# Performance work log

Hardware: AMD Instinct MI355X
Metric: run time of the kernel (lower is better)

## Reference

```python
import jax, jax.numpy as jnp
import numpy as np

H = 768
NH = 12
HD = H // NH
FF = 3072
EPS = 1e-5
CHUNK = 32  # query chunk for L1 distance to bound memory


def layer_norm(x, g, b):
    mu = jnp.mean(x, axis=-1, keepdims=True)
    var = jnp.mean((x - mu) ** 2, axis=-1, keepdims=True)
    return (x - mu) / jnp.sqrt(var + EPS) * g + b


def l1_distance(Q, K):
    # Q, K: [BH, S, D] -> [BH, S, S], computed in query chunks to avoid
    # materializing the full [BH, S, S, D] broadcast intermediate.
    BH, S, D = Q.shape
    nc = S // CHUNK
    Qc = Q.reshape(BH, nc, CHUNK, D).transpose(1, 0, 2, 3)  # [nc, BH, c, D]

    def f(qc):  # qc: [BH, c, D]
        return jnp.sum(jnp.abs(qc[:, :, None, :] - K[:, None, :, :]), axis=-1)

    d = jax.lax.map(f, Qc)  # [nc, BH, c, S]
    return d.transpose(1, 0, 2, 3).reshape(BH, S, S)


def setup_inputs() -> dict:
    key = jax.random.key(0)
    ks = jax.random.split(key, 12)
    sd = 0.02
    B, S = 2, 1024
    return {
        'hidden_states': jax.random.normal(ks[0], (B, S, H), jnp.float32),
        'ln1_g': jnp.ones((H,), jnp.float32),
        'ln1_b': jnp.zeros((H,), jnp.float32),
        'Wq': jax.random.normal(ks[1], (H, H), jnp.float32) * sd,
        'bq': jnp.zeros((H,), jnp.float32),
        'Wk': jax.random.normal(ks[2], (H, H), jnp.float32) * sd,
        'bk': jnp.zeros((H,), jnp.float32),
        'Wv': jax.random.normal(ks[3], (H, H), jnp.float32) * sd,
        'bv': jnp.zeros((H,), jnp.float32),
        'Wo': jax.random.normal(ks[4], (H, H), jnp.float32) * sd,
        'bo': jnp.zeros((H,), jnp.float32),
        'lam': jnp.asarray(1.0, jnp.float32),
        'ln2_g': jnp.ones((H,), jnp.float32),
        'ln2_b': jnp.zeros((H,), jnp.float32),
        'W1': jax.random.normal(ks[5], (H, FF), jnp.float32) * sd,
        'b1': jnp.zeros((FF,), jnp.float32),
        'W2': jax.random.normal(ks[6], (FF, H), jnp.float32) * sd,
        'b2': jnp.zeros((H,), jnp.float32),
    }


def reference(hidden_states, ln1_g, ln1_b, Wq, bq, Wk, bk, Wv, bv, Wo, bo,
              lam, ln2_g, ln2_b, W1, b1, W2, b2):
    B, S, _ = hidden_states.shape
    scale = 1.0 / np.sqrt(HD)

    residual = hidden_states
    x = layer_norm(hidden_states, ln1_g, ln1_b)

    Q = (x @ Wq + bq).reshape(B, S, NH, HD).transpose(0, 2, 1, 3)  # [B,H,S,D]
    K = (x @ Wk + bk).reshape(B, S, NH, HD).transpose(0, 2, 1, 3)
    V = (x @ Wv + bv).reshape(B, S, NH, HD).transpose(0, 2, 1, 3)

    Qf = Q.reshape(B * NH, S, HD)
    Kf = K.reshape(B * NH, S, HD)
    dist = l1_distance(Qf, Kf).reshape(B, NH, S, S)

    scores = -lam * dist * scale
    attn = jax.nn.softmax(scores, axis=-1)  # [B,H,S,S]

    out = jnp.einsum('bhqk,bhkd->bhqd', attn, V)
    out = out.transpose(0, 2, 1, 3).reshape(B, S, H)
    out = out @ Wo + bo
    out = residual + out

    residual = out
    y = layer_norm(out, ln2_g, ln2_b)
    y = jax.nn.gelu(y @ W1 + b1, approximate=False) @ W2 + b2
    out = residual + y
    return out, attn
```

## Files before the change

### kernel.cpp

```cpp
#include <hip/hip_runtime.h>
#include <cstdint>
#include <cstddef>

#define SB    1024
#define BB    2
#define HH    768
#define NHH   12
#define HDD   64
#define FFF   3072
#define RR    (BB*SB)
#define NQKV  2304

#define QSCALE 42.5f

typedef __attribute__((ext_vector_type(8))) short short8;
typedef __attribute__((ext_vector_type(4))) float f4;

__device__ __forceinline__ unsigned short f2bf(float f) {
  union { float f; unsigned u; } x; x.f = f;
  unsigned r = x.u + 0x7FFFu + ((x.u >> 16) & 1u);
  return (unsigned short)(r >> 16);
}

__device__ __forceinline__ unsigned qz8(float x) {
  int v = (int)rintf(x * QSCALE) + 128;
  v = v < 0 ? 0 : (v > 255 ? 255 : v);
  return (unsigned)v;
}

__device__ __forceinline__ void async16(void* lds, const void* g) {
  __builtin_amdgcn_global_load_lds((const __attribute__((address_space(1))) unsigned int*)g,
                                   (__attribute__((address_space(3))) unsigned int*)lds,
                                   16, 0, 0);
}

__global__ __launch_bounds__(256)
void prep_all(const float* __restrict__ Wq, const float* __restrict__ Wk,
              const float* __restrict__ Wv, const float* __restrict__ Wo,
              const float* __restrict__ W1, const float* __restrict__ W2,
              const float* __restrict__ bq, const float* __restrict__ bk,
              const float* __restrict__ bv,
              const float* __restrict__ hidden, const float* __restrict__ ln1_g,
              const float* __restrict__ ln1_b,
              unsigned short* __restrict__ Wqkv_t, unsigned short* __restrict__ W1t,
              unsigned short* __restrict__ W2t, float* __restrict__ bqkv,
              unsigned short* __restrict__ xb) {
  const int t = blockIdx.x;
  const int tid = threadIdx.x;
  __shared__ float tile[64][65];
  __shared__ float rs[4], rq[4];
  if (t >= 1737) {
    const int row = t - 1737;
    const float* x = hidden + (size_t)row * HH;
    float v0 = x[tid], v1 = x[tid + 256], v2 = x[tid + 512];
    float s = v0 + v1 + v2;
    float q = v0 * v0 + v1 * v1 + v2 * v2;
    #pragma unroll
    for (int o = 32; o >= 1; o >>= 1) { s += __shfl_xor(s, o); q += __shfl_xor(q, o); }
    const int w = tid >> 6;
    if ((tid & 63) == 0) { rs[w] = s; rq[w] = q; }
    __syncthreads();
    s = rs[0] + rs[1] + rs[2] + rs[3];
    q = rq[0] + rq[1] + rq[2] + rq[3];
    float mean = s * (1.0f / HH);
    float rstd = rsqrtf(q * (1.0f / HH) - mean * mean + 1e-5f);
    unsigned short* o0 = xb + (size_t)row * HH;
    o0[tid]       = f2bf((v0 - mean) * rstd * ln1_g[tid]       + ln1_b[tid]);
    o0[tid + 256] = f2bf((v1 - mean) * rstd * ln1_g[tid + 256] + ln1_b[tid + 256]);
    o0[tid + 512] = f2bf((v2 - mean) * rstd * ln1_g[tid + 512] + ln1_b[tid + 512]);
    return;
  }
  if (t >= 1728) {
    int i = (t - 1728) * 256 + tid;
    if (i < NQKV)
      bqkv[i] = (i < HH) ? bq[i] : (i < 2 * HH ? bk[i - HH] : bv[i - 2 * HH]);
    return;
  }
  const float* in; unsigned short* out; int ldin, ldout, r0, c0;
  if (t < 576) {
    int m = t / 144, q = t % 144;
    in = m == 0 ? Wq : (m == 1 ? Wk : (m == 2 ? Wv : Wo));
    out = Wqkv_t + (size_t)m * HH * HH;
    ldin = HH; ldout = HH;
    r0 = (q / 12) * 64; c0 = (q % 12) * 64;
  } else if (t < 1152) {
    int q = t - 576;
    in = W1; out = W1t; ldin = FFF; ldout = HH;
    r0 = (q % 12) * 64; c0 = (q / 12) * 64;
  } else {
    int q = t - 1152;
    in = W2; out = W2t; ldin = HH; ldout = FFF;
    r0 = (q % 48) * 64; c0 = (q / 48) * 64;
  }
  for (int i = tid; i < 4096; i += 256) {
    int r = i >> 6, c = i & 63;
    tile[r][c] = in[(size_t)(r0 + r) * ldin + c0 + c];
  }
  __syncthreads();
  for (int i = tid; i < 4096; i += 256) {
    int cc = i >> 6, rr = i & 63;
    out[(size_t)(c0 + cc) * ldout + r0 + rr] = f2bf(tile[rr][cc]);
  }
}

__global__ __launch_bounds__(256)
void gemm_qkv(const unsigned short* __restrict__ A, const unsigned short* __restrict__ Bt,
              const float* __restrict__ bqkv, unsigned* __restrict__ Qq,
              unsigned* __restrict__ Kq, unsigned short* __restrict__ Vt) {
  __shared__ __align__(16) unsigned char smem[49152];
  unsigned short (*lA)[128 * 32] = (unsigned short (*)[128 * 32])smem;
  unsigned short (*lB)[128 * 32] = (unsigned short (*)[128 * 32])(smem + 24576);
  const unsigned short* Ab = A + (size_t)blockIdx.y * 128 * HH;
  const unsigned short* Bb = Bt + (size_t)blockIdx.x * 128 * HH;
  const int tid = threadIdx.x;
  const int wave = tid >> 6, lane = tid & 63;
  const int wr = wave >> 1, wc = wave & 1;
  const int lo = lane & 15, hi = lane >> 4;

  auto stage = [&](int k0, int buf) {
    #pragma unroll
    for (int i = 0; i < 512; i += 256) {
      int idx = i + tid; int r = idx >> 2, kg = idx & 3;
      async16(&lA[buf][idx * 8], &Ab[(size_t)r * HH + k0 + kg * 8]);
    }
    #pragma unroll
    for (int i = 0; i < 512; i += 256) {
      int idx = i + tid; int r = idx >> 2, kg = idx & 3;
      async16(&lB[buf][idx * 8], &Bb[(size_t)r * HH + k0 + kg * 8]);
    }
  };

  stage(0, 0);
  stage(32, 1);
  f4 acc[4][4] = {};
  for (int it = 0; it < 24; it++) {
    if (it + 1 < 24) {
      asm volatile("s_waitcnt vmcnt(4)" ::: "memory");
    } else {
      asm volatile("s_waitcnt vmcnt(0)" ::: "memory");
    }
    __builtin_amdgcn_s_barrier();
    __builtin_amdgcn_sched_barrier(0);
    const int cur = it % 3;
    short8 af[4], bf[4];
    #pragma unroll
    for (int i = 0; i < 4; i++)
      af[i] = *(const short8*)&lA[cur][(wr * 64 + i * 16 + lo) * 32 + hi * 8];
    #pragma unroll
    for (int j = 0; j < 4; j++)
      bf[j] = *(const short8*)&lB[cur][(wc * 64 + j * 16 + lo) * 32 + hi * 8];
    if (it + 2 < 24) stage((it + 2) * 32, (it + 2) % 3);
    #pragma unroll
    for (int i = 0; i < 4; i++)
      #pragma unroll
      for (int j = 0; j < 4; j++)
        acc[i][j] = __builtin_amdgcn_mfma_f32_16x16x32_bf16(af[i], bf[j], acc[i][j], 0, 0, 0);
  }
  __syncthreads();

  const int reg = blockIdx.x / 6;
  const int cb = blockIdx.x * 128;
  if (reg < 2) {
    unsigned char* t8 = smem;
    #pragma unroll
    for (int i = 0; i < 4; i++)
      #pragma unroll
      for (int j = 0; j < 4; j++) {
        int col = wc * 64 + j * 16 + lo;
        float bv_ = bqkv[cb + col];
        #pragma unroll
        for (int r = 0; r < 4; r++) {
          int row = wr * 64 + i * 16 + hi * 4 + r;
          t8[row * 132 + col] = (unsigned char)qz8(acc[i][j][r] + bv_);
        }
      }
    __syncthreads();
    const unsigned* t32 = (const unsigned*)smem;
    if (reg == 0) {
      #pragma unroll
      for (int i0 = 0; i0 < 4096; i0 += 256) {
        int idx = i0 + tid;
        int cw = idx & 31, rw = idx >> 5;
        int token = blockIdx.y * 128 + rw;
        Qq[(size_t)token * 192 + blockIdx.x * 32 + cw] = t32[rw * 33 + cw];
      }
    } else {
      #pragma unroll
      for (int i0 = 0; i0 < 4096; i0 += 256) {
        int idx = i0 + tid;
        int rw = idx & 127, cw = idx >> 7;
        int token = blockIdx.y * 128 + rw;
        int b = token >> 10, k = token & 1023;
        int dgG = (blockIdx.x - 6) * 32 + cw;
        Kq[(size_t)((b * NHH + (dgG >> 4)) * 16 + (dgG & 15)) * SB + k] = t32[rw * 33 + cw];
      }
    }
  } else {
    unsigned short* t16 = (unsigned short*)smem;
    #pragma unroll
    for (int i = 0; i < 4; i++)
      #pragma unroll
      for (int j = 0; j < 4; j++) {
        int col = wc * 64 + j * 16 + lo;
        float bv_ = bqkv[cb + col];
        #pragma unroll
        for (int r = 0; r < 4; r++) {
          int row = wr * 64 + i * 16 + hi * 4 + r;
          t16[col * 130 + row] = f2bf(acc[i][j][r] + bv_);
        }
      }
    __syncthreads();
    const unsigned* tv = (const unsigned*)smem;
    unsigned* VtU = (unsigned*)Vt;
    #pragma unroll
    for (int i0 = 0; i0 < 8192; i0 += 256) {
      int idx = i0 + tid;
      int rp = idx & 63, cw = idx >> 6;
      int gcol = (blockIdx.x - 12) * 128 + cw;
      int h = gcol >> 6, d = gcol & 63;
      int b = blockIdx.y >> 3;
      VtU[(size_t)((b * NHH + h) * HDD + d) * 512 + (blockIdx.y & 7) * 64 + rp] =
          tv[cw * 65 + rp];
    }
  }
}

template<int BM, int BN, int WR, int WC, int MODE, int KS>
__global__ __launch_bounds__(WR*WC*64)
void gemm_bt(const unsigned short* __restrict__ A, int ldA,
             const unsigned short* __restrict__ Bt, int ldB,
             void* __restrict__ Cv, int ldC,
             const float* __restrict__ bias,
             int K, long partStride) {
  constexpr int T = WR * WC * 64;
  constexpr int LPT = (BM * 4 + BN * 4) / T;
  __shared__ unsigned short lA[3][BM * 32];
  __shared__ unsigned short lB[3][BN * 32];
  const int ks = blockIdx.z;
  const int KH = K / KS;
  const unsigned short* Ab = A + (size_t)blockIdx.y * BM * ldA + (size_t)ks * KH;
  const unsigned short* Bb = Bt + (size_t)blockIdx.x * BN * ldB + (size_t)ks * KH;
  const long cOff = (long)blockIdx.y * BM * ldC + (long)blockIdx.x * BN
                  + (long)ks * partStride;
  const int tid = threadIdx.x;
  const int wave = tid >> 6, lane = tid & 63;
  const int wr = wave / WC, wc = wave % WC;
  const int lo = lane & 15, hi = lane >> 4;

  auto stage = [&](int k0, int buf) {
    #pragma unroll
    for (int i = 0; i < BM * 4; i += T) {
      int idx = i + tid; int r = idx >> 2, kg = idx & 3;
      async16(&lA[buf][idx * 8], &Ab[(size_t)r * ldA + k0 + kg * 8]);
    }
    #pragma unroll
    for (int i = 0; i < BN * 4; i += T) {
      int idx = i + tid; int r = idx >> 2, kg = idx & 3;
      async16(&lB[buf][idx * 8], &Bb[(size_t)r * ldB + k0 + kg * 8]);
    }
  };

  const int nIter = KH / 32;
  stage(0, 0);
  if (nIter > 1) stage(32, 1);
  f4 acc[4][4] = {};
  for (int it = 0; it < nIter; it++) {
    if (it + 1 < nIter) {
      asm volatile("s_waitcnt vmcnt(%0)" :: "n"(LPT) : "memory");
    } else {
      asm volatile("s_waitcnt vmcnt(0)" ::: "memory");
    }
    __builtin_amdgcn_s_barrier();
    __builtin_amdgcn_sched_barrier(0);
    const int cur = it % 3;
    short8 af[4], bf[4];
    #pragma unroll
    for (int i = 0; i < 4; i++)
      af[i] = *(const short8*)&lA[cur][(wr * 64 + i * 16 + lo) * 32 + hi * 8];
    #pragma unroll
    for (int j = 0; j < 4; j++)
      bf[j] = *(const short8*)&lB[cur][(wc * 64 + j * 16 + lo) * 32 + hi * 8];
    if (it + 2 < nIter) stage((it + 2) * 32, (it + 2) % 3);
    #pragma unroll
    for (int i = 0; i < 4; i++)
      #pragma unroll
      for (int j = 0; j < 4; j++)
        acc[i][j] = __builtin_amdgcn_mfma_f32_16x16x32_bf16(af[i], bf[j], acc[i][j], 0, 0, 0);
  }
  float* Cf = (float*)Cv;
  unsigned short* Cb = (unsigned short*)Cv;
  const int bc0 = blockIdx.x * BN;
  #pragma unroll
  for (int i = 0; i < 4; i++) {
    #pragma unroll
    for (int j = 0; j < 4; j++) {
      int col = wc * 64 + j * 16 + lo;
      #pragma unroll
      for (int r = 0; r < 4; r++) {
        int row = wr * 64 + i * 16 + hi * 4 + r;
        size_t idx = (size_t)cOff + (size_t)row * ldC + col;
        float v = acc[i][j][r];
        if constexpr (MODE == 3) {
          float tt = v + bias[bc0 + col];
          Cb[idx] = f2bf(0.5f * tt * (1.0f + erff(tt * 0.70710678118654752f)));
        } else {
          Cf[idx] = v;
        }
      }
    }
  }
}

__global__ __launch_bounds__(256)
void reduce_ln(const float* __restrict__ p, const float* __restrict__ bias,
               const float* __restrict__ res, const float* __restrict__ g,
               const float* __restrict__ bb, float* __restrict__ attnOut,
               unsigned short* __restrict__ out) {
  const int row = blockIdx.x, tid = threadIdx.x;
  const size_t rb = (size_t)row * HH;
  float v[3]; float s = 0.f, q = 0.f;
  #pragma unroll
  for (int j = 0; j < 3; j++) {
    int c = tid + j * 256;
    size_t idx = rb + c;
    float a = p[idx] + p[(size_t)RR * HH + idx] + p[2 * (size_t)RR * HH + idx]
            + p[3 * (size_t)RR * HH + idx] + bias[c] + res[idx];
    attnOut[idx] = a;
    v[j] = a; s += a; q += a * a;
  }
  #pragma unroll
  for (int o = 32; o >= 1; o >>= 1) { s += __shfl_xor(s, o); q += __shfl_xor(q, o); }
  __shared__ float rs[4], rq[4];
  const int w = tid >> 6;
  if ((tid & 63) == 0) { rs[w] = s; rq[w] = q; }
  __syncthreads();
  s = rs[0] + rs[1] + rs[2] + rs[3];
  q = rq[0] + rq[1] + rq[2] + rq[3];
  float mean = s * (1.0f / HH);
  float rstd = rsqrtf(q * (1.0f / HH) - mean * mean + 1e-5f);
  #pragma unroll
  for (int j = 0; j < 3; j++) {
    int c = tid + j * 256;
    out[rb + c] = f2bf((v[j] - mean) * rstd * g[c] + bb[c]);
  }
}

__global__ __launch_bounds__(256)
void reduce4_bias_res(const float* __restrict__ p, const float* __restrict__ bias,
                      const float* __restrict__ res, float* __restrict__ out) {
  int i = (blockIdx.x * 256 + threadIdx.x) * 4;
  int col = i % HH;
  float4 a = *(const float4*)(p + i);
  #pragma unroll
  for (int s = 1; s < 4; s++) {
    float4 b = *(const float4*)(p + (size_t)s * RR * HH + i);
    a.x += b.x; a.y += b.y; a.z += b.z; a.w += b.w;
  }
  float4 bb = *(const float4*)(bias + col);
  float4 r = *(const float4*)(res + i);
  float4 o;
  o.x = a.x + bb.x + r.x;
  o.y = a.y + bb.y + r.y;
  o.z = a.z + bb.z + r.z;
  o.w = a.w + bb.w + r.w;
  *(float4*)(out + i) = o;
}

#define DQ 16
__global__ __launch_bounds__(512)
void dist_softmax_pv(const unsigned* __restrict__ Qq, const unsigned* __restrict__ Kq,
                     const unsigned short* __restrict__ Vt,
                     const float* __restrict__ lam_p,
                     float* __restrict__ attnF, unsigned short* __restrict__ ctx) {
  __shared__ __align__(16) unsigned lk[8 * SB];
  __shared__ unsigned lq[DQ * 16];
  const int bh = blockIdx.y;
  const int q0 = blockIdx.x * DQ;
  const int b = bh / NHH, h = bh % NHH;
  const int tid = threadIdx.x;
  const int w = tid >> 6, lane = tid & 63;
  const int lo = lane & 15, hi = lane >> 4;

  if (tid < 256) {
    int r = tid >> 4, dg = tid & 15;
    lq[r * 16 + dg] = Qq[(size_t)(b * SB + q0 + r) * 192 + h * 16 + dg];
  }

  const unsigned* Ks = Kq + (size_t)bh * 16 * SB;
  unsigned acc[2][4][4] = {};
  const unsigned* lqw = &lq[(w * 2) * 16];

  #pragma unroll
  for (int ch = 0; ch < 2; ch++) {
    #pragma unroll
    for (int i = 0; i < 4; i++)
      async16(&lk[(i * 512 + tid) * 4], Ks + (size_t)ch * 8192 + (i * 512 + tid) * 4);
    __syncthreads();
    #pragma unroll
    for (int dg = 0; dg < 8; dg++) {
      unsigned qd[2];
      #pragma unroll
      for (int qi = 0; qi < 2; qi++) qd[qi] = lqw[qi * 16 + ch * 8 + dg];
      uint4 kv[4];
      #pragma unroll
      for (int kg = 0; kg < 4; kg++)
        kv[kg] = *(const uint4*)&lk[dg * SB + kg * 256 + lane * 4];
      #pragma unroll
      for (int qi = 0; qi < 2; qi++) {
        #pragma unroll
        for (int kg = 0; kg < 4; kg++) {
          acc[qi][kg][0] = __builtin_amdgcn_sad_u8(qd[qi], kv[kg].x, acc[qi][kg][0]);
          acc[qi][kg][1] = __builtin_amdgcn_sad_u8(qd[qi], kv[kg].y, acc[qi][kg][1]);
          acc[qi][kg][2] = __builtin_amdgcn_sad_u8(qd[qi], kv[kg].z, acc[qi][kg][2]);
          acc[qi][kg][3] = __builtin_amdgcn_sad_u8(qd[qi], kv[kg].w, acc[qi][kg][3]);
        }
      }
    }
    __syncthreads();
  }

  unsigned short* lp = (unsigned short*)lk;
  const float kscl = -lam_p[0] * 0.125f / QSCALE;
  #pragma unroll
  for (int qi = 0; qi < 2; qi++) {
    float sc[16];
    float m = -1e30f;
    #pragma unroll
    for (int kg = 0; kg < 4; kg++)
      #pragma unroll
      for (int c = 0; c < 4; c++) {
        float v = (float)acc[qi][kg][c] * kscl;
        sc[kg * 4 + c] = v;
        m = fmaxf(m, v);
      }
    #pragma unroll
    for (int off = 1; off < 64; off <<= 1) m = fmaxf(m, __shfl_xor(m, off));
    float s = 0.f;
    #pragma unroll
    for (int i = 0; i < 16; i++) {
      float e = __expf(sc[i] - m);
      sc[i] = e;
      s += e;
    }
    #pragma unroll
    for (int off = 1; off < 64; off <<= 1) s += __shfl_xor(s, off);
    const float rinv = 1.0f / s;
    const int row = w * 2 + qi;
    const size_t gb = (size_t)bh * SB * SB + (size_t)(q0 + row) * SB + lane * 4;
    #pragma unroll
    for (int kg = 0; kg < 4; kg++) {
      float4 p;
      p.x = sc[kg * 4 + 0] * rinv;
      p.y = sc[kg * 4 + 1] * rinv;
      p.z = sc[kg * 4 + 2] * rinv;
      p.w = sc[kg * 4 + 3] * rinv;
      *(float4*)&attnF[gb + kg * 256] = p;
      ushort4 pb;
      pb.x = f2bf(p.x); pb.y = f2bf(p.y); pb.z = f2bf(p.z); pb.w = f2bf(p.w);
      *(ushort4*)&lp[row * SB + kg * 256 + lane * 4] = pb;
    }
  }
  __syncthreads();

  if (w < 4) {
    const unsigned short* Vb = Vt + ((size_t)bh * HDD + w * 16 + lo) * SB + hi * 8;
    const unsigned short* Pb = lp + lo * SB + hi * 8;
    f4 cacc = {0.f, 0.f, 0.f, 0.f};
    #pragma unroll
    for (int k0 = 0; k0 < SB; k0 += 32) {
      short8 af = *(const short8*)(Pb + k0);
      short8 bf = *(const short8*)(Vb + k0);
      cacc = __builtin_amdgcn_mfma_f32_16x16x32_bf16(af, bf, cacc, 0, 0, 0);
    }
    unsigned short* cb = ctx + (size_t)(b * SB + q0 + hi * 4) * HH + h * HDD + w * 16 + lo;
    #pragma unroll
    for (int r = 0; r < 4; r++) cb[(size_t)r * HH] = f2bf(cacc[r]);
  }
}

extern "C" void kernel_launch(void* const* d_in, const int* in_sizes, int n_in,
                              void* d_out, int out_size, void* d_ws, size_t ws_size,
                              hipStream_t stream) {
  (void)in_sizes; (void)n_in; (void)out_size; (void)ws_size;
  const float* hidden = (const float*)d_in[0];
  const float* ln1_g  = (const float*)d_in[1];
  const float* ln1_b  = (const float*)d_in[2];
  const float* Wq     = (const float*)d_in[3];
  const float* bq     = (const float*)d_in[4];
  const float* Wk     = (const float*)d_in[5];
  const float* bk     = (const float*)d_in[6];
  const float* Wv     = (const float*)d_in[7];
  const float* bv     = (const float*)d_in[8];
  const float* Wo     = (const float*)d_in[9];
  const float* bo     = (const float*)d_in[10];
  const float* lam    = (const float*)d_in[11];
  const float* ln2_g  = (const float*)d_in[12];
  const float* ln2_b  = (const float*)d_in[13];
  const float* W1     = (const float*)d_in[14];
  const float* b1     = (const float*)d_in[15];
  const float* W2     = (const float*)d_in[16];
  const float* b2     = (const float*)d_in[17];

  float* out0  = (float*)d_out;
  float* attnF = out0 + (size_t)RR * HH;

  char* w = (char*)d_ws;
  auto alloc = [&](size_t bytes) { char* p = w; w += (bytes + 255) & ~(size_t)255; return p; };
  unsigned short* xb      = (unsigned short*)alloc((size_t)RR * HH * 2);
  unsigned short* Wqkv_t  = (unsigned short*)alloc((size_t)NQKV * HH * 2);
  unsigned short* Wo_t    = (unsigned short*)alloc((size_t)HH * HH * 2);
  unsigned short* W1t     = (unsigned short*)alloc((size_t)FFF * HH * 2);
  unsigned short* W2t     = (unsigned short*)alloc((size_t)HH * FFF * 2);
  float*          bqkv    = (float*)alloc((size_t)NQKV * 4);
  unsigned*       Qq      = (unsigned*)alloc((size_t)RR * 192 * 4);
  unsigned*       Kq      = (unsigned*)alloc((size_t)BB * NHH * 16 * SB * 4);
  unsigned short* Vt      = (unsigned short*)alloc((size_t)BB * NHH * HDD * SB * 2);
  unsigned short* ctx     = (unsigned short*)alloc((size_t)RR * HH * 2);
  float*          attnOut = (float*)alloc((size_t)RR * HH * 4);
  unsigned short* h1      = (unsigned short*)alloc((size_t)RR * FFF * 2);
  float*          gPart   = (float*)alloc((size_t)4 * RR * HH * 4);
  unsigned short* y2      = Vt;
  (void)Wo_t;

  prep_all<<<dim3(1737 + RR), 256, 0, stream>>>(Wq, Wk, Wv, Wo, W1, W2, bq, bk, bv,
                                                hidden, ln1_g, ln1_b,
                                                Wqkv_t, W1t, W2t, bqkv, xb);

  gemm_qkv<<<dim3(NQKV / 128, RR / 128), 256, 0, stream>>>(
      xb, Wqkv_t, bqkv, Qq, Kq, Vt);

  dist_softmax_pv<<<dim3(SB / DQ, BB * NHH), 512, 0, stream>>>(
      Qq, Kq, Vt, lam, attnF, ctx);

  gemm_bt<128, 128, 2, 2, 4, 4><<<dim3(HH / 128, RR / 128, 4), 256, 0, stream>>>(
      ctx, HH, Wqkv_t + (size_t)3 * HH * HH, HH, gPart, HH,
      nullptr, HH, (long)RR * HH);

  reduce_ln<<<dim3(RR), 256, 0, stream>>>(gPart, bo, hidden, ln2_g, ln2_b,
                                          attnOut, y2);

  gemm_bt<128, 128, 2, 2, 3, 1><<<dim3(FFF / 128, RR / 128, 1), 256, 0, stream>>>(
      y2, HH, W1t, HH, h1, FFF, b1, HH, 0);

  gemm_bt<128, 128, 2, 2, 4, 4><<<dim3(HH / 128, RR / 128, 4), 256, 0, stream>>>(
      h1, FFF, W2t, FFF, gPart, HH, nullptr, FFF, (long)RR * HH);

  reduce4_bias_res<<<dim3(RR * HH / 1024), 256, 0, stream>>>(gPart, b2, attnOut, out0);
}
```

Measured before the change: 283.5 us.

## Replace split-K partial buffers and reduction kernels with atomic accumulation into outputs

Result: slower. 302.0 us (+6.5%).

```diff
diff --git a/kernel.cpp b/kernel.cpp
--- a/kernel.cpp
+++ b/kernel.cpp
@@ -39,12 +39,12 @@
               const float* __restrict__ Wv, const float* __restrict__ Wo,
               const float* __restrict__ W1, const float* __restrict__ W2,
               const float* __restrict__ bq, const float* __restrict__ bk,
-              const float* __restrict__ bv,
+              const float* __restrict__ bv, const float* __restrict__ bo,
               const float* __restrict__ hidden, const float* __restrict__ ln1_g,
               const float* __restrict__ ln1_b,
               unsigned short* __restrict__ Wqkv_t, unsigned short* __restrict__ W1t,
               unsigned short* __restrict__ W2t, float* __restrict__ bqkv,
-              unsigned short* __restrict__ xb) {
+              unsigned short* __restrict__ xb, float* __restrict__ attnOut) {
   const int t = blockIdx.x;
   const int tid = threadIdx.x;
   __shared__ float tile[64][65];
@@ -53,6 +53,10 @@
     const int row = t - 1737;
     const float* x = hidden + (size_t)row * HH;
     float v0 = x[tid], v1 = x[tid + 256], v2 = x[tid + 512];
+    float* ao = attnOut + (size_t)row * HH;
+    ao[tid]       = v0 + bo[tid];
+    ao[tid + 256] = v1 + bo[tid + 256];
+    ao[tid + 512] = v2 + bo[tid + 512];
     float s = v0 + v1 + v2;
     float q = v0 * v0 + v1 * v1 + v2 * v2;
     #pragma unroll
@@ -231,7 +235,7 @@
              const unsigned short* __restrict__ Bt, int ldB,
              void* __restrict__ Cv, int ldC,
              const float* __restrict__ bias,
-             int K, long partStride) {
+             int K) {
   constexpr int T = WR * WC * 64;
   constexpr int LPT = (BM * 4 + BN * 4) / T;
   __shared__ unsigned short lA[3][BM * 32];
@@ -240,8 +244,7 @@
   const int KH = K / KS;
   const unsigned short* Ab = A + (size_t)blockIdx.y * BM * ldA + (size_t)ks * KH;
   const unsigned short* Bb = Bt + (size_t)blockIdx.x * BN * ldB + (size_t)ks * KH;
-  const long cOff = (long)blockIdx.y * BM * ldC + (long)blockIdx.x * BN
-                  + (long)ks * partStride;
+  const long cOff = (long)blockIdx.y * BM * ldC + (long)blockIdx.x * BN;
   const int tid = threadIdx.x;
   const int wave = tid >> 6, lane = tid & 63;
   const int wr = wave / WC, wc = wave % WC;
@@ -304,7 +307,7 @@
           float tt = v + bias[bc0 + col];
           Cb[idx] = f2bf(0.5f * tt * (1.0f + erff(tt * 0.70710678118654752f)));
         } else {
-          Cf[idx] = v;
+          atomicAdd(&Cf[idx], v);
         }
       }
     }
@@ -312,22 +315,18 @@
 }
 
 __global__ __launch_bounds__(256)
-void reduce_ln(const float* __restrict__ p, const float* __restrict__ bias,
-               const float* __restrict__ res, const float* __restrict__ g,
-               const float* __restrict__ bb, float* __restrict__ attnOut,
-               unsigned short* __restrict__ out) {
+void ln_b2(const float* __restrict__ attnOut, const float* __restrict__ g,
+           const float* __restrict__ bb, const float* __restrict__ b2,
+           unsigned short* __restrict__ y2, float* __restrict__ out0) {
   const int row = blockIdx.x, tid = threadIdx.x;
   const size_t rb = (size_t)row * HH;
-  float v[3]; float s = 0.f, q = 0.f;
-  #pragma unroll
-  for (int j = 0; j < 3; j++) {
-    int c = tid + j * 256;
-    size_t idx = rb + c;
-    float a = p[idx] + p[(size_t)RR * HH + idx] + p[2 * (size_t)RR * HH + idx]
-            + p[3 * (size_t)RR * HH + idx] + bias[c] + res[idx];
-    attnOut[idx] = a;
-    v[j] = a; s += a; q += a * a;
-  }
+  const float* x = attnOut + rb;
+  float v0 = x[tid], v1 = x[tid + 256], v2 = x[tid + 512];
+  out0[rb + tid]       = v0 + b2[tid];
+  out0[rb + tid + 256] = v1 + b2[tid + 256];
+  out0[rb + tid + 512] = v2 + b2[tid + 512];
+  float s = v0 + v1 + v2;
+  float q = v0 * v0 + v1 * v1 + v2 * v2;
   #pragma unroll
   for (int o = 32; o >= 1; o >>= 1) { s += __shfl_xor(s, o); q += __shfl_xor(q, o); }
   __shared__ float rs[4], rq[4];
@@ -338,32 +337,10 @@
   q = rq[0] + rq[1] + rq[2] + rq[3];
   float mean = s * (1.0f / HH);
   float rstd = rsqrtf(q * (1.0f / HH) - mean * mean + 1e-5f);
-  #pragma unroll
-  for (int j = 0; j < 3; j++) {
-    int c = tid + j * 256;
-    out[rb + c] = f2bf((v[j] - mean) * rstd * g[c] + bb[c]);
-  }
-}
-
-__global__ __launch_bounds__(256)
-void reduce4_bias_res(const float* __restrict__ p, const float* __restrict__ bias,
-                      const float* __restrict__ res, float* __restrict__ out) {
-  int i = (blockIdx.x * 256 + threadIdx.x) * 4;
-  int col = i % HH;
-  float4 a = *(const float4*)(p + i);
-  #pragma unroll
-  for (int s = 1; s < 4; s++) {
-    float4 b = *(const float4*)(p + (size_t)s * RR * HH + i);
-    a.x += b.x; a.y += b.y; a.z += b.z; a.w += b.w;
-  }
-  float4 bb = *(const float4*)(bias + col);
-  float4 r = *(const float4*)(res + i);
-  float4 o;
-  o.x = a.x + bb.x + r.x;
-  o.y = a.y + bb.y + r.y;
-  o.z = a.z + bb.z + r.z;
-  o.w = a.w + bb.w + r.w;
-  *(float4*)(out + i) = o;
+  unsigned short* o0 = y2 + rb;
+  o0[tid]       = f2bf((v0 - mean) * rstd * g[tid]       + bb[tid]);
+  o0[tid + 256] = f2bf((v1 - mean) * rstd * g[tid + 256] + bb[tid + 256]);
+  o0[tid + 512] = f2bf((v2 - mean) * rstd * g[tid + 512] + bb[tid + 512]);
 }
 
 #define DQ 16
@@ -518,13 +495,13 @@
   unsigned short* ctx     = (unsigned short*)alloc((size_t)RR * HH * 2);
   float*          attnOut = (float*)alloc((size_t)RR * HH * 4);
   unsigned short* h1      = (unsigned short*)alloc((size_t)RR * FFF * 2);
-  float*          gPart   = (float*)alloc((size_t)4 * RR * HH * 4);
   unsigned short* y2      = Vt;
   (void)Wo_t;
 
-  prep_all<<<dim3(1737 + RR), 256, 0, stream>>>(Wq, Wk, Wv, Wo, W1, W2, bq, bk, bv,
+  prep_all<<<dim3(1737 + RR), 256, 0, stream>>>(Wq, Wk, Wv, Wo, W1, W2,
+                                                bq, bk, bv, bo,
                                                 hidden, ln1_g, ln1_b,
-                                                Wqkv_t, W1t, W2t, bqkv, xb);
+                                                Wqkv_t, W1t, W2t, bqkv, xb, attnOut);
 
   gemm_qkv<<<dim3(NQKV / 128, RR / 128), 256, 0, stream>>>(
       xb, Wqkv_t, bqkv, Qq, Kq, Vt);
@@ -532,18 +509,14 @@
   dist_softmax_pv<<<dim3(SB / DQ, BB * NHH), 512, 0, stream>>>(
       Qq, Kq, Vt, lam, attnF, ctx);
 
-  gemm_bt<128, 128, 2, 2, 4, 4><<<dim3(HH / 128, RR / 128, 4), 256, 0, stream>>>(
-      ctx, HH, Wqkv_t + (size_t)3 * HH * HH, HH, gPart, HH,
-      nullptr, HH, (long)RR * HH);
-
-  reduce_ln<<<dim3(RR), 256, 0, stream>>>(gPart, bo, hidden, ln2_g, ln2_b,
-                                          attnOut, y2);
+  gemm_bt<128, 128, 2, 2, 5, 4><<<dim3(HH / 128, RR / 128, 4), 256, 0, stream>>>(
+      ctx, HH, Wqkv_t + (size_t)3 * HH * HH, HH, attnOut, HH, nullptr, HH);
+
+  ln_b2<<<dim3(RR), 256, 0, stream>>>(attnOut, ln2_g, ln2_b, b2, y2, out0);
 
   gemm_bt<128, 128, 2, 2, 3, 1><<<dim3(FFF / 128, RR / 128, 1), 256, 0, stream>>>(
-      y2, HH, W1t, HH, h1, FFF, b1, HH, 0);
-
-  gemm_bt<128, 128, 2, 2, 4, 4><<<dim3(HH / 128, RR / 128, 4), 256, 0, stream>>>(
-      h1, FFF, W2t, FFF, gPart, HH, nullptr, FFF, (long)RR * HH);
-
-  reduce4_bias_res<<<dim3(RR * HH / 1024), 256, 0, stream>>>(gPart, b2, attnOut, out0);
-}
+      y2, HH, W1t, HH, h1, FFF, b1, HH);
+
+  gemm_bt<128, 128, 2, 2, 5, 4><<<dim3(HH / 128, RR / 128, 4), 256, 0, stream>>>(
+      h1, FFF, W2t, FFF, out0, HH, nullptr, FFF);
+}
```

## Read K directly from global in L1 distance and XOR-swizzle P in LDS

Applied to the files above, without the earlier changes.

New measurement: 294.5 us. +3.9%, slower.

```diff
diff --git a/kernel.cpp b/kernel.cpp
--- a/kernel.cpp
+++ b/kernel.cpp
@@ -372,7 +372,7 @@
                      const unsigned short* __restrict__ Vt,
                      const float* __restrict__ lam_p,
                      float* __restrict__ attnF, unsigned short* __restrict__ ctx) {
-  __shared__ __align__(16) unsigned lk[8 * SB];
+  __shared__ __align__(16) unsigned short lp[DQ * SB];
   __shared__ unsigned lq[DQ * 16];
   const int bh = blockIdx.y;
   const int q0 = blockIdx.x * DQ;
@@ -385,41 +385,33 @@
     int r = tid >> 4, dg = tid & 15;
     lq[r * 16 + dg] = Qq[(size_t)(b * SB + q0 + r) * 192 + h * 16 + dg];
   }
+  __syncthreads();
 
   const unsigned* Ks = Kq + (size_t)bh * 16 * SB;
   unsigned acc[2][4][4] = {};
   const unsigned* lqw = &lq[(w * 2) * 16];
 
   #pragma unroll
-  for (int ch = 0; ch < 2; ch++) {
-    #pragma unroll
-    for (int i = 0; i < 4; i++)
-      async16(&lk[(i * 512 + tid) * 4], Ks + (size_t)ch * 8192 + (i * 512 + tid) * 4);
-    __syncthreads();
-    #pragma unroll
-    for (int dg = 0; dg < 8; dg++) {
-      unsigned qd[2];
-      #pragma unroll
-      for (int qi = 0; qi < 2; qi++) qd[qi] = lqw[qi * 16 + ch * 8 + dg];
-      uint4 kv[4];
-      #pragma unroll
-      for (int kg = 0; kg < 4; kg++)
-        kv[kg] = *(const uint4*)&lk[dg * SB + kg * 256 + lane * 4];
-      #pragma unroll
-      for (int qi = 0; qi < 2; qi++) {
-        #pragma unroll
-        for (int kg = 0; kg < 4; kg++) {
-          acc[qi][kg][0] = __builtin_amdgcn_sad_u8(qd[qi], kv[kg].x, acc[qi][kg][0]);
-          acc[qi][kg][1] = __builtin_amdgcn_sad_u8(qd[qi], kv[kg].y, acc[qi][kg][1]);
-          acc[qi][kg][2] = __builtin_amdgcn_sad_u8(qd[qi], kv[kg].z, acc[qi][kg][2]);
-          acc[qi][kg][3] = __builtin_amdgcn_sad_u8(qd[qi], kv[kg].w, acc[qi][kg][3]);
-        }
-      }
-    }
-    __syncthreads();
-  }
-
-  unsigned short* lp = (unsigned short*)lk;
+  for (int dg = 0; dg < 16; dg++) {
+    unsigned qd0 = lqw[dg];
+    unsigned qd1 = lqw[16 + dg];
+    uint4 kv[4];
+    #pragma unroll
+    for (int kg = 0; kg < 4; kg++)
+      kv[kg] = *(const uint4*)&Ks[(size_t)dg * SB + kg * 256 + lane * 4];
+    #pragma unroll
+    for (int kg = 0; kg < 4; kg++) {
+      acc[0][kg][0] = __builtin_amdgcn_sad_u8(qd0, kv[kg].x, acc[0][kg][0]);
+      acc[0][kg][1] = __builtin_amdgcn_sad_u8(qd0, kv[kg].y, acc[0][kg][1]);
+      acc[0][kg][2] = __builtin_amdgcn_sad_u8(qd0, kv[kg].z, acc[0][kg][2]);
+      acc[0][kg][3] = __builtin_amdgcn_sad_u8(qd0, kv[kg].w, acc[0][kg][3]);
+      acc[1][kg][0] = __builtin_amdgcn_sad_u8(qd1, kv[kg].x, acc[1][kg][0]);
+      acc[1][kg][1] = __builtin_amdgcn_sad_u8(qd1, kv[kg].y, acc[1][kg][1]);
+      acc[1][kg][2] = __builtin_amdgcn_sad_u8(qd1, kv[kg].z, acc[1][kg][2]);
+      acc[1][kg][3] = __builtin_amdgcn_sad_u8(qd1, kv[kg].w, acc[1][kg][3]);
+    }
+  }
+
   const float kscl = -lam_p[0] * 0.125f / QSCALE;
   #pragma unroll
   for (int qi = 0; qi < 2; qi++) {
@@ -446,6 +438,7 @@
     for (int off = 1; off < 64; off <<= 1) s += __shfl_xor(s, off);
     const float rinv = 1.0f / s;
     const int row = w * 2 + qi;
+    const unsigned swz = (unsigned)((row & 7) << 3);
     const size_t gb = (size_t)bh * SB * SB + (size_t)(q0 + row) * SB + lane * 4;
     #pragma unroll
     for (int kg = 0; kg < 4; kg++) {
@@ -457,18 +450,19 @@
       *(float4*)&attnF[gb + kg * 256] = p;
       ushort4 pb;
       pb.x = f2bf(p.x); pb.y = f2bf(p.y); pb.z = f2bf(p.z); pb.w = f2bf(p.w);
-      *(ushort4*)&lp[row * SB + kg * 256 + lane * 4] = pb;
+      *(ushort4*)&lp[(unsigned)(row * SB + kg * 256 + lane * 4) ^ swz] = pb;
     }
   }
   __syncthreads();
 
   if (w < 4) {
     const unsigned short* Vb = Vt + ((size_t)bh * HDD + w * 16 + lo) * SB + hi * 8;
-    const unsigned short* Pb = lp + lo * SB + hi * 8;
+    const unsigned pswz = (unsigned)((lo & 7) << 3);
+    const unsigned pbase = (unsigned)(lo * SB + hi * 8);
     f4 cacc = {0.f, 0.f, 0.f, 0.f};
     #pragma unroll
     for (int k0 = 0; k0 < SB; k0 += 32) {
-      short8 af = *(const short8*)(Pb + k0);
+      short8 af = *(const short8*)&lp[(pbase + k0) ^ pswz];
       short8 bf = *(const short8*)(Vb + k0);
       cacc = __builtin_amdgcn_mfma_f32_16x16x32_bf16(af, bf, cacc, 0, 0, 0);
     }
```
